# Kernel optimization log

Measured on AMD Instinct MI355X. Metric: run time of the kernel, lower is better.

The kernel has to match this reference:

```python
import jax, jax.numpy as jnp
import numpy as np

EPS_L2 = 1e-6
EPS_RMS = 1e-6

def _dw_causal(x, w):
    # depthwise causal conv: x [B,L,C], w [C,K] (torch Conv1d weight [C,1,K] squeezed)
    K = w.shape[1]
    L = x.shape[1]
    xp = jnp.pad(x, ((0, 0), (K - 1, 0), (0, 0)))
    out = jnp.zeros_like(x)
    for j in range(K):  # K=4, fixed small kernel
        out = out + w[:, j] * xp[:, j:j + L, :]
    return out

def _qkv_conv(x, dw, pw):
    # depthwise causal conv -> pointwise 1x1 conv -> SiLU
    return jax.nn.silu(_dw_causal(x, dw) @ pw.T)

def _l2n(x):
    return x / (jnp.linalg.norm(x, axis=-1, keepdims=True) + EPS_L2)

def setup_inputs() -> dict:
    key = jax.random.key(0)
    B, L, D, M, P, K = 2, 1024, 2048, 2048, 8, 4
    ks = jax.random.split(key, 16)
    inp = {}
    inp['x'] = jax.random.normal(ks[0], (B, L, D), dtype=jnp.float32)
    inp['Wq'] = jax.random.normal(ks[1], (M, D), dtype=jnp.float32) * 0.02
    inp['Wk'] = jax.random.normal(ks[2], (M, D), dtype=jnp.float32) * 0.02
    inp['Wv'] = jax.random.normal(ks[3], (M, D), dtype=jnp.float32) * 0.02
    inp['q_dw'] = jax.random.normal(ks[4], (M, K), dtype=jnp.float32) * 0.1
    inp['k_dw'] = jax.random.normal(ks[5], (M, K), dtype=jnp.float32) * 0.1
    inp['v_dw'] = jax.random.normal(ks[6], (M, K), dtype=jnp.float32) * 0.1
    inp['q_pw'] = jax.random.normal(ks[7], (M, M), dtype=jnp.float32) * 0.02
    inp['k_pw'] = jax.random.normal(ks[8], (M, M), dtype=jnp.float32) * 0.02
    inp['v_pw'] = jax.random.normal(ks[9], (M, M), dtype=jnp.float32) * 0.02
    inp['pk'] = jax.random.normal(ks[10], (P, M), dtype=jnp.float32) * 0.02
    inp['pv'] = jax.random.normal(ks[11], (P, M), dtype=jnp.float32) * 0.02
    inp['mlp_w1'] = jnp.eye(M, dtype=jnp.float32) * 0.1
    inp['mlp_w2'] = jnp.eye(M, dtype=jnp.float32) * 0.1
    inp['eta_w'] = jnp.zeros((1, D), dtype=jnp.float32)
    inp['eta_b'] = jnp.full((1,), 2.0, dtype=jnp.float32)
    inp['theta_w'] = jnp.zeros((1, D), dtype=jnp.float32)
    inp['theta_b'] = jnp.full((1,), -1.0, dtype=jnp.float32)
    inp['alpha_w'] = jnp.zeros((1, D), dtype=jnp.float32)
    inp['alpha_b'] = jnp.full((1,), -2.0, dtype=jnp.float32)
    inp['gate_w'] = jax.random.normal(ks[12], (M, M), dtype=jnp.float32) * 0.02
    inp['gate_b'] = jnp.zeros((M,), dtype=jnp.float32)
    inp['out_w'] = jax.random.normal(ks[13], (D, M), dtype=jnp.float32) * 0.02
    inp['ln_w'] = jnp.ones((D,), dtype=jnp.float32)
    inp['mem_state'] = jnp.zeros((M, M), dtype=jnp.float32)
    inp['sur_state'] = jnp.zeros((M, M), dtype=jnp.float32)
    return inp

def reference(x, Wq, Wk, Wv, q_dw, q_pw, k_dw, k_pw, v_dw, v_pw, pk, pv,
              mlp_w1, mlp_w2, eta_w, eta_b, theta_w, theta_b, alpha_w, alpha_b,
              gate_w, gate_b, out_w, ln_w, mem_state, sur_state):
    B, L, D = x.shape
    M = Wq.shape[0]
    P = pk.shape[0]
    # projections + causal depthwise-separable convs + SiLU
    q = _qkv_conv(x @ Wq.T, q_dw, q_pw)
    k = _qkv_conv(x @ Wk.T, k_dw, k_pw)
    v = _qkv_conv(x @ Wv.T, v_dw, v_pw)
    q = _l2n(q)
    k = _l2n(k)
    # data-dependent eta/theta/alpha from mean-pooled input, scalarized
    x_pooled = x.mean(axis=1)  # [B, D]
    eta = jax.nn.sigmoid(x_pooled @ eta_w.T + eta_b).mean()
    theta = jax.nn.sigmoid(x_pooled @ theta_w.T + theta_b).mean()
    alpha = jax.nn.sigmoid(x_pooled @ alpha_w.T + alpha_b).mean()
    # persistent memory tokens
    pk_n = _l2n(pk)
    k_wp = jnp.concatenate([jnp.broadcast_to(pk_n[None], (B, P, M)), k], axis=1)
    v_wp = jnp.concatenate([jnp.broadcast_to(pv[None], (B, P, M)), v], axis=1)
    # test-time memory update (torch.no_grad block -> stop_gradient)
    pred = jnp.einsum('blm,mh->blh', k, mem_state)
    err = v - pred
    momentary = jnp.einsum('bld,blh->dh', k, err) / (B * L)
    new_surprise = eta * sur_state + theta * momentary
    new_memory = (1.0 - alpha) * mem_state + new_surprise
    snapshot = jax.lax.stop_gradient(new_memory)
    # retrieval: linear memory + deep memory MLP
    linear_ret = jnp.einsum('blm,mh->blh', q, snapshot)
    mlp_ret = jax.nn.silu(q @ mlp_w1.T) @ mlp_w2.T
    retrieved = linear_ret + mlp_ret
    # causal attention with always-visible persistent tokens
    scores = jnp.einsum('blm,bpm->blp', q, k_wp) / jnp.sqrt(jnp.float32(M))
    col = jnp.arange(P + L)
    row = jnp.arange(L)
    mask = (col[None, :] < P) | ((col[None, :] - P) <= row[:, None])  # [L, P+L]
    scores = jnp.where(mask[None], scores, -jnp.inf)
    attn = jax.nn.softmax(scores.astype(jnp.float32), axis=-1).astype(x.dtype)
    context = jnp.einsum('blp,bpm->blm', attn, v_wp)
    retrieved = retrieved + context
    # gated output projection + residual + RMSNorm
    gate = jax.nn.sigmoid(retrieved @ gate_w.T + gate_b)
    out = x + (gate * retrieved) @ out_w.T
    rms = jnp.sqrt(jnp.mean(out * out, axis=-1, keepdims=True) + EPS_RMS)
    return (out / rms) * ln_w
```

## Files before the change

### kernel.cpp

```cpp
#include <hip/hip_runtime.h>
#include <hip/hip_bf16.h>


#define NROWS 2048
#define MD    2048
#define PL    1032
#define PLP   1152
#define NM    4194304

using bf16x8 = __attribute__((ext_vector_type(8))) __bf16;
using f32x4  = __attribute__((ext_vector_type(4))) float;
using u16x8  = __attribute__((ext_vector_type(8))) unsigned short;

__device__ __forceinline__ unsigned short f2bf(float f) {
    union { float f; unsigned int u; } c; c.f = f;
    unsigned int u = c.u;
    return (unsigned short)((u + 0x7fffu + ((u >> 16) & 1u)) >> 16);
}
__device__ __forceinline__ float bf2f(unsigned short h) {
    union { float f; unsigned int u; } c; c.u = ((unsigned int)h) << 16;
    return c.f;
}
__device__ __forceinline__ float ldf(const float* p) { return *p; }
__device__ __forceinline__ float ldf(const unsigned short* p) { return bf2f(*p); }
__device__ __forceinline__ float sigm(float x) { return 1.f / (1.f + __expf(-x)); }
__device__ __forceinline__ float silu(float x) { return x / (1.f + __expf(-x)); }

__device__ __forceinline__ float block_reduce_sum(float v) {
    __shared__ float ws[4];
    #pragma unroll
    for (int o = 32; o > 0; o >>= 1) v += __shfl_down(v, o);
    __syncthreads();
    if ((threadIdx.x & 63) == 0) ws[threadIdx.x >> 6] = v;
    __syncthreads();
    return (ws[0] + ws[1]) + (ws[2] + ws[3]);
}
__device__ __forceinline__ float block_reduce_max(float v) {
    __shared__ float wm[4];
    #pragma unroll
    for (int o = 32; o > 0; o >>= 1) v = fmaxf(v, __shfl_down(v, o));
    __syncthreads();
    if ((threadIdx.x & 63) == 0) wm[threadIdx.x >> 6] = v;
    __syncthreads();
    return fmaxf(fmaxf(wm[0], wm[1]), fmaxf(wm[2], wm[3]));
}

__device__ __forceinline__ void load_lds16(const unsigned short* g, unsigned short* l) {
    __builtin_amdgcn_global_load_lds(
        (const __attribute__((address_space(1))) unsigned int*)g,
        (__attribute__((address_space(3))) unsigned int*)l, 16, 0, 0);
}
__device__ __forceinline__ void raw_barrier() {
    __asm__ volatile("" ::: "memory");
    __builtin_amdgcn_s_barrier();
    __asm__ volatile("" ::: "memory");
}
__device__ __forceinline__ void epi_store(int epi, float* Cf, unsigned short* Ch,
                                          long off, float v) {
    if (epi == 0)      Cf[off] = v;
    else if (epi == 1) Cf[off] += v;
    else if (epi == 2) Ch[off] = f2bf(v);
    else               Ch[off] = f2bf(silu(v));
}

__global__ __launch_bounds__(256) void gemm_nt(
    const unsigned short* __restrict__ A, const unsigned short* __restrict__ Bm,
    void* __restrict__ Cv, int Mc, int K, long sA, long sB, long sCb, int epiPack)
{
    __shared__ unsigned short As[2][8192];
    __shared__ unsigned short Bs[2][4096];
    const int tid = threadIdx.x, lane = tid & 63, w = tid >> 6;
    const int l16 = lane & 15, quad = lane >> 4;
    const int wr = (w >> 1) * 64, wc = (w & 1) * 32;
    const long rowBase = (long)blockIdx.y * 128;
    const long colBase = (long)blockIdx.x * 64;
    const unsigned short* Ap = A + (long)blockIdx.z * sA;
    const unsigned short* Bp = Bm + (long)blockIdx.z * sB;
    const int epi = (epiPack >> (blockIdx.z * 4)) & 15;
    const int r8 = lane >> 3;
    const int cg = (lane & 7) ^ r8;

    const unsigned short* gA[4]; const unsigned short* gB[2];
    unsigned short* lA[4]; unsigned short* lB[2];
    #pragma unroll
    for (int t = 0; t < 4; ++t) {
        int ch = w * 4 + t;
        gA[t] = Ap + (rowBase + ch * 8 + r8) * (long)K + cg * 8;
        lA[t] = &As[0][ch * 512];
    }
    #pragma unroll
    for (int t = 0; t < 2; ++t) {
        int ch = w * 2 + t;
        gB[t] = Bp + (colBase + ch * 8 + r8) * (long)K + cg * 8;
        lB[t] = &Bs[0][ch * 512];
    }

    f32x4 acc[4][2] = {};
    #pragma unroll
    for (int t = 0; t < 4; ++t) { load_lds16(gA[t], lA[t]); gA[t] += 64; }
    #pragma unroll
    for (int t = 0; t < 2; ++t) { load_lds16(gB[t], lB[t]); gB[t] += 64; }

    const int nIter = K >> 6;
    for (int it = 0; it < nIter; ++it) {
        const int cb = it & 1;
        if (it + 1 < nIter) {
            const int nb = cb ^ 1;
            #pragma unroll
            for (int t = 0; t < 4; ++t) { load_lds16(gA[t], lA[t] + nb * 8192); gA[t] += 64; }
            #pragma unroll
            for (int t = 0; t < 2; ++t) { load_lds16(gB[t], lB[t] + nb * 4096); gB[t] += 64; }
            __builtin_amdgcn_s_waitcnt(0xF76);
        } else {
            __builtin_amdgcn_s_waitcnt(0xF70);
        }
        raw_barrier();
        const unsigned short* Ac = As[cb];
        const unsigned short* Bc = Bs[cb];
        #pragma unroll
        for (int ks = 0; ks < 2; ++ks) {
            const int cl = ((ks * 4 + quad) ^ (l16 & 7)) * 8;
            bf16x8 af[4], bfr[2];
            #pragma unroll
            for (int i = 0; i < 4; ++i)
                af[i] = *(const bf16x8*)&Ac[(wr + i * 16 + l16) * 64 + cl];
            #pragma unroll
            for (int j = 0; j < 2; ++j)
                bfr[j] = *(const bf16x8*)&Bc[(wc + j * 16 + l16) * 64 + cl];
            #pragma unroll
            for (int i = 0; i < 4; ++i)
                #pragma unroll
                for (int j = 0; j < 2; ++j)
                    acc[i][j] = __builtin_amdgcn_mfma_f32_16x16x32_bf16(af[i], bfr[j], acc[i][j], 0, 0, 0);
        }
        raw_barrier();
    }

    char* Cb = (char*)Cv + (long)blockIdx.z * sCb;
    float* Cf = (float*)Cb;
    unsigned short* Ch = (unsigned short*)Cb;
    #pragma unroll
    for (int i = 0; i < 4; ++i)
        #pragma unroll
        for (int r = 0; r < 4; ++r) {
            long gr = rowBase + wr + i * 16 + quad * 4 + r;
            #pragma unroll
            for (int j = 0; j < 2; ++j) {
                long gc = colBase + wc + j * 16 + l16;
                epi_store(epi, Cf, Ch, gr * (long)Mc + gc, acc[i][j][r]);
            }
        }
}

__global__ __launch_bounds__(256) void gemm_nt_big(
    const unsigned short* __restrict__ A, const unsigned short* __restrict__ Bm,
    void* __restrict__ Cv, int Mc, int K, long sA, long sB, long sCb, int epiPack)
{
    __shared__ unsigned short As[2][8192];
    __shared__ unsigned short Bs[2][8192];
    const int tid = threadIdx.x, lane = tid & 63, w = tid >> 6;
    const int l16 = lane & 15, quad = lane >> 4;
    const int wr = (w >> 1) * 64, wc = (w & 1) * 64;
    const long rowBase = (long)blockIdx.y * 128;
    const long colBase = (long)blockIdx.x * 128;
    const unsigned short* Ap = A + (long)blockIdx.z * sA;
    const unsigned short* Bp = Bm + (long)blockIdx.z * sB;
    const int epi = (epiPack >> (blockIdx.z * 4)) & 15;
    const int r8 = lane >> 3;
    const int cg = (lane & 7) ^ r8;

    const unsigned short* gA[4]; const unsigned short* gB[4];
    unsigned short* lA[4]; unsigned short* lB[4];
    #pragma unroll
    for (int t = 0; t < 4; ++t) {
        int ch = w * 4 + t;
        gA[t] = Ap + (rowBase + ch * 8 + r8) * (long)K + cg * 8;
        lA[t] = &As[0][ch * 512];
        gB[t] = Bp + (colBase + ch * 8 + r8) * (long)K + cg * 8;
        lB[t] = &Bs[0][ch * 512];
    }

    f32x4 acc[4][4] = {};
    #pragma unroll
    for (int t = 0; t < 4; ++t) { load_lds16(gA[t], lA[t]); gA[t] += 64; }
    #pragma unroll
    for (int t = 0; t < 4; ++t) { load_lds16(gB[t], lB[t]); gB[t] += 64; }

    const int nIter = K >> 6;
    for (int it = 0; it < nIter; ++it) {
        const int cb = it & 1;
        if (it + 1 < nIter) {
            const int nb = cb ^ 1;
            #pragma unroll
            for (int t = 0; t < 4; ++t) { load_lds16(gA[t], lA[t] + nb * 8192); gA[t] += 64; }
            #pragma unroll
            for (int t = 0; t < 4; ++t) { load_lds16(gB[t], lB[t] + nb * 8192); gB[t] += 64; }
            __builtin_amdgcn_s_waitcnt(0xF78);
        } else {
            __builtin_amdgcn_s_waitcnt(0xF70);
        }
        raw_barrier();
        const unsigned short* Ac = As[cb];
        const unsigned short* Bc = Bs[cb];
        #pragma unroll
        for (int ks = 0; ks < 2; ++ks) {
            const int cl = ((ks * 4 + quad) ^ (l16 & 7)) * 8;
            bf16x8 af[4], bfr[4];
            #pragma unroll
            for (int i = 0; i < 4; ++i)
                af[i] = *(const bf16x8*)&Ac[(wr + i * 16 + l16) * 64 + cl];
            #pragma unroll
            for (int j = 0; j < 4; ++j)
                bfr[j] = *(const bf16x8*)&Bc[(wc + j * 16 + l16) * 64 + cl];
            #pragma unroll
            for (int i = 0; i < 4; ++i)
                #pragma unroll
                for (int j = 0; j < 4; ++j)
                    acc[i][j] = __builtin_amdgcn_mfma_f32_16x16x32_bf16(af[i], bfr[j], acc[i][j], 0, 0, 0);
        }
        raw_barrier();
    }

    char* Cb = (char*)Cv + (long)blockIdx.z * sCb;
    float* Cf = (float*)Cb;
    unsigned short* Ch = (unsigned short*)Cb;
    #pragma unroll
    for (int i = 0; i < 4; ++i)
        #pragma unroll
        for (int r = 0; r < 4; ++r) {
            long gr = rowBase + wr + i * 16 + quad * 4 + r;
            #pragma unroll
            for (int j = 0; j < 4; ++j) {
                long gc = colBase + wc + j * 16 + l16;
                epi_store(epi, Cf, Ch, gr * (long)Mc + gc, acc[i][j][r]);
            }
        }
}

template <typename TS>
__global__ void k_transpose(const TS* __restrict__ src, unsigned short* __restrict__ dst,
                            int R, int C, int dstLd, int dstOff, long sSrc, long sDst)
{
    __shared__ float tile[32][33];
    const TS* sp = src + (long)blockIdx.z * sSrc;
    unsigned short* dp = dst + (long)blockIdx.z * sDst;
    int c0 = blockIdx.x * 32, r0 = blockIdx.y * 32;
    int tx = threadIdx.x, ty = threadIdx.y;
    #pragma unroll
    for (int i = 0; i < 4; ++i)
        tile[ty + i * 8][tx] = ldf(&sp[(long)(r0 + ty + i * 8) * C + c0 + tx]);
    __syncthreads();
    #pragma unroll
    for (int i = 0; i < 4; ++i)
        dp[(long)(c0 + ty + i * 8) * dstLd + dstOff + r0 + tx] = f2bf(tile[tx][ty + i * 8]);
}

__global__ void k_errT_kT(const unsigned short* __restrict__ vf, const float* __restrict__ pred,
                          const unsigned short* __restrict__ k_bf, unsigned short* __restrict__ eT)
{
    __shared__ float tile[32][33];
    int z = blockIdx.z;
    int c0 = blockIdx.x * 32, r0 = blockIdx.y * 32;
    int tx = threadIdx.x, ty = threadIdx.y;
    #pragma unroll
    for (int i = 0; i < 4; ++i) {
        long idx = (long)(r0 + ty + i * 8) * MD + c0 + tx;
        tile[ty + i * 8][tx] = (z == 0) ? (bf2f(vf[idx]) - pred[idx]) : bf2f(k_bf[idx]);
    }
    __syncthreads();
    unsigned short* dst = eT + (long)z * NM;
    #pragma unroll
    for (int i = 0; i < 4; ++i)
        dst[(long)(c0 + ty + i * 8) * MD + r0 + tx] = f2bf(tile[tx][ty + i * 8]);
}

__global__ void k_snapT(const float* __restrict__ mem, const float* __restrict__ sur,
                        const float* __restrict__ momT, const float* __restrict__ scal,
                        unsigned short* __restrict__ dst)
{
    __shared__ float tile[32][33];
    float eta = scal[0], theta = scal[1], alpha = scal[2];
    int h0 = blockIdx.y * 32, d0 = blockIdx.x * 32;
    int tx = threadIdx.x, ty = threadIdx.y;
    #pragma unroll
    for (int i = 0; i < 4; ++i) {
        long idx = (long)(d0 + ty + i * 8) * MD + h0 + tx;
        tile[ty + i * 8][tx] = (1.f - alpha) * mem[idx] + eta * sur[idx];
    }
    __syncthreads();
    #pragma unroll
    for (int i = 0; i < 4; ++i) {
        long oidx = (long)(h0 + ty + i * 8) * MD + d0 + tx;
        dst[oidx] = f2bf(tile[tx][ty + i * 8] + theta * (1.f / 2048.f) * momT[oidx]);
    }
}

__global__ void k_cvt_multi(const float* s0, const float* s1, const float* s2, const float* s3,
                            const float* s4, const float* s5, const float* s6, const float* s7,
                            unsigned short* d0, unsigned short* d1, unsigned short* d2, unsigned short* d3,
                            unsigned short* d4, unsigned short* d5, unsigned short* d6, unsigned short* d7)
{
    int seg = blockIdx.x >> 11;
    const float* s; unsigned short* d;
    switch (seg) {
        case 0: s = s0; d = d0; break;  case 1: s = s1; d = d1; break;
        case 2: s = s2; d = d2; break;  case 3: s = s3; d = d3; break;
        case 4: s = s4; d = d4; break;  case 5: s = s5; d = d5; break;
        case 6: s = s6; d = d6; break;  default: s = s7; d = d7; break;
    }
    long idx = ((long)(blockIdx.x & 2047) * 256 + threadIdx.x) * 8;
    float4 a = *(const float4*)(s + idx);
    float4 b = *(const float4*)(s + idx + 4);
    u16x8 o;
    o[0] = f2bf(a.x); o[1] = f2bf(a.y); o[2] = f2bf(a.z); o[3] = f2bf(a.w);
    o[4] = f2bf(b.x); o[5] = f2bf(b.y); o[6] = f2bf(b.z); o[7] = f2bf(b.w);
    *(u16x8*)(d + idx) = o;
}

__global__ void k_dwconv(const unsigned short* __restrict__ tproj,
                         const float* __restrict__ qdw, const float* __restrict__ kdw,
                         const float* __restrict__ vdw, unsigned short* __restrict__ conv)
{
    long u = (long)blockIdx.x * 256 + threadIdx.x;
    long flat = u * 8;
    int z = (int)(flat >> 22);
    int rem = (int)(flat & (NM - 1));
    int n = rem >> 11, m = rem & 2047;
    int l = n & 1023;
    const float* dw = (z == 0) ? qdw : (z == 1) ? kdw : vdw;
    const unsigned short* src = tproj + (long)n * 6144 + z * 2048 + m;
    float4 dwv[8];
    #pragma unroll
    for (int e = 0; e < 8; ++e) dwv[e] = *(const float4*)(dw + (m + e) * 4);
    float acc[8] = {};
    #pragma unroll
    for (int j = 0; j < 4; ++j) {
        int dl = j - 3;
        if (l + dl >= 0) {
            u16x8 r = *(const u16x8*)(src + (long)dl * 6144);
            #pragma unroll
            for (int e = 0; e < 8; ++e)
                acc[e] += ((const float*)&dwv[e])[j] * bf2f(r[e]);
        }
    }
    u16x8 o;
    #pragma unroll
    for (int e = 0; e < 8; ++e) o[e] = f2bf(acc[e]);
    *(u16x8*)(conv + (long)z * NM + (long)n * 2048 + m) = o;
}

__global__ void k_post_qkv(const float* __restrict__ t_big, unsigned short* __restrict__ q_bf,
                           unsigned short* __restrict__ k_bf, unsigned short* __restrict__ vf,
                           unsigned short* __restrict__ kwp)
{
    int bid = blockIdx.x, z = bid >> 11, n = bid & 2047;
    const float* row = t_big + (long)z * NM + (long)n * 2048;
    int t = threadIdx.x;
    float4 a = *(const float4*)(row + t * 8);
    float4 b = *(const float4*)(row + t * 8 + 4);
    float v[8] = {silu(a.x), silu(a.y), silu(a.z), silu(a.w),
                  silu(b.x), silu(b.y), silu(b.z), silu(b.w)};
    if (z == 2) {
        u16x8 o;
        #pragma unroll
        for (int e = 0; e < 8; ++e) o[e] = f2bf(v[e]);
        *(u16x8*)(vf + (long)n * 2048 + t * 8) = o;
        return;
    }
    float ss = 0.f;
    #pragma unroll
    for (int e = 0; e < 8; ++e) ss += v[e] * v[e];
    ss = block_reduce_sum(ss);
    float inv = 1.f / (sqrtf(ss) + 1e-6f);
    u16x8 o;
    #pragma unroll
    for (int e = 0; e < 8; ++e) o[e] = f2bf(v[e] * inv);
    if (z == 0) {
        *(u16x8*)(q_bf + (long)n * 2048 + t * 8) = o;
    } else {
        *(u16x8*)(k_bf + (long)n * 2048 + t * 8) = o;
        int bb = n >> 10, l = n & 1023;
        *(u16x8*)(kwp + ((long)bb * PLP + 8 + l) * MD + t * 8) = o;
    }
}

__global__ void k_misc(const float* __restrict__ pk, const float* __restrict__ pv,
                       unsigned short* __restrict__ kwp, unsigned short* __restrict__ vwpT)
{
    int bid = blockIdx.x, t = threadIdx.x;
    if (bid < 8) {
        const float* row = pk + bid * MD;
        float4 a = *(const float4*)(row + t * 8);
        float4 b = *(const float4*)(row + t * 8 + 4);
        float v[8] = {a.x, a.y, a.z, a.w, b.x, b.y, b.z, b.w};
        float ss = 0.f;
        #pragma unroll
        for (int e = 0; e < 8; ++e) ss += v[e] * v[e];
        ss = block_reduce_sum(ss);
        float inv = 1.f / (sqrtf(ss) + 1e-6f);
        u16x8 o;
        #pragma unroll
        for (int e = 0; e < 8; ++e) o[e] = f2bf(v[e] * inv);
        *(u16x8*)(kwp + (long)bid * MD + t * 8) = o;
        *(u16x8*)(kwp + (long)PLP * MD + (long)bid * MD + t * 8) = o;
    } else if (bid < 72) {
        int i = (bid - 8) * 256 + t;
        int m = i >> 3, pp = i & 7;
        unsigned short h = f2bf(pv[pp * MD + m]);
        vwpT[(long)m * PLP + pp] = h;
        vwpT[(long)MD * PLP + (long)m * PLP + pp] = h;
    } else if (bid < 312) {
        long flat = ((long)(bid - 72) * 256 + t) * 8;
        int b = (int)(flat / 245760);
        int r = (int)(flat % 245760);
        int j = 1032 + (r >> 11), m = r & 2047;
        u16x8 zz = {};
        *(u16x8*)(kwp + ((long)b * PLP + j) * MD + m) = zz;
    } else {
        long flat = ((long)(bid - 312) * 256 + t) * 8;
        int bm = (int)(flat / 120);
        int o = (int)(flat % 120);
        u16x8 zz = {};
        *(u16x8*)(vwpT + (long)bm * PLP + 1032 + o) = zz;
    }
}

__global__ void k_pooled(const float* __restrict__ x, const float* __restrict__ ew,
                         const float* __restrict__ tw, const float* __restrict__ aw,
                         float* __restrict__ dots) {
    int b = blockIdx.y;
    long base = (long)b * 1024 * MD;
    long start = (long)blockIdx.x * 8192;
    float s0 = 0, s1 = 0, s2 = 0;
    for (int s = 0; s < 32; ++s) {
        long f = start + threadIdx.x + (long)s * 256;
        float xv = x[base + f];
        int d = (int)(f & (MD - 1));
        s0 += xv * ew[d]; s1 += xv * tw[d]; s2 += xv * aw[d];
    }
    s0 = block_reduce_sum(s0);
    if (threadIdx.x == 0) atomicAdd(&dots[0 + b], s0);
    s1 = block_reduce_sum(s1);
    if (threadIdx.x == 0) atomicAdd(&dots[2 + b], s1);
    s2 = block_reduce_sum(s2);
    if (threadIdx.x == 0) atomicAdd(&dots[4 + b], s2);
}
__global__ void k_scal_fin(const float* __restrict__ dots, const float* __restrict__ eb,
                           const float* __restrict__ tb, const float* __restrict__ ab,
                           float* __restrict__ scal) {
    if (threadIdx.x == 0 && blockIdx.x == 0) {
        const float invL = 1.f / 1024.f;
        float e = 0, th = 0, al = 0;
        for (int b = 0; b < 2; ++b) {
            e  += sigm(dots[0 + b] * invL + eb[0]);
            th += sigm(dots[2 + b] * invL + tb[0]);
            al += sigm(dots[4 + b] * invL + ab[0]);
        }
        scal[0] = e * 0.5f; scal[1] = th * 0.5f; scal[2] = al * 0.5f;
    }
}

__global__ void k_addcvt(const float* __restrict__ a, const float* __restrict__ b,
                         unsigned short* __restrict__ o) {
    long i = ((long)blockIdx.x * 256 + threadIdx.x) * 8;
    float4 a0 = *(const float4*)(a + i), a1 = *(const float4*)(a + i + 4);
    float4 b0 = *(const float4*)(b + i), b1 = *(const float4*)(b + i + 4);
    u16x8 r;
    r[0] = f2bf(a0.x + b0.x); r[1] = f2bf(a0.y + b0.y); r[2] = f2bf(a0.z + b0.z); r[3] = f2bf(a0.w + b0.w);
    r[4] = f2bf(a1.x + b1.x); r[5] = f2bf(a1.y + b1.y); r[6] = f2bf(a1.z + b1.z); r[7] = f2bf(a1.w + b1.w);
    *(u16x8*)(o + i) = r;
}
__global__ void k_gate8(const float* __restrict__ pre, const float* __restrict__ gb,
                        const float* __restrict__ ret, const float* __restrict__ mlp2,
                        unsigned short* __restrict__ o) {
    long i = ((long)blockIdx.x * 256 + threadIdx.x) * 8;
    int m = (int)(i & (MD - 1));
    float4 p0 = *(const float4*)(pre + i),  p1 = *(const float4*)(pre + i + 4);
    float4 r0 = *(const float4*)(ret + i),  r1 = *(const float4*)(ret + i + 4);
    float4 q0 = *(const float4*)(mlp2 + i), q1 = *(const float4*)(mlp2 + i + 4);
    float4 g0 = *(const float4*)(gb + m),   g1 = *(const float4*)(gb + m + 4);
    u16x8 r;
    r[0] = f2bf(sigm(p0.x + g0.x) * (r0.x + q0.x));
    r[1] = f2bf(sigm(p0.y + g0.y) * (r0.y + q0.y));
    r[2] = f2bf(sigm(p0.z + g0.z) * (r0.z + q0.z));
    r[3] = f2bf(sigm(p0.w + g0.w) * (r0.w + q0.w));
    r[4] = f2bf(sigm(p1.x + g1.x) * (r1.x + q1.x));
    r[5] = f2bf(sigm(p1.y + g1.y) * (r1.y + q1.y));
    r[6] = f2bf(sigm(p1.z + g1.z) * (r1.z + q1.z));
    r[7] = f2bf(sigm(p1.w + g1.w) * (r1.w + q1.w));
    *(u16x8*)(o + i) = r;
}

__global__ void k_softmax(const float* __restrict__ S, unsigned short* __restrict__ attn) {
    int l = blockIdx.x, b = blockIdx.y;
    long base = ((long)b * 1024 + l) * PLP;
    int nvis = 8 + l + 1;
    const float scale = 0.022097086912079608f;
    int t = threadIdx.x;
    float vals[5];
    float mx = -1e30f;
    #pragma unroll
    for (int s = 0; s < 5; ++s) {
        int j = t + s * 256;
        float v = -1e30f;
        if (j < nvis) v = S[base + j] * scale;
        vals[s] = v;
        mx = fmaxf(mx, v);
    }
    mx = block_reduce_max(mx);
    float sum = 0.f;
    #pragma unroll
    for (int s = 0; s < 5; ++s) {
        int j = t + s * 256;
        float e = 0.f;
        if (j < nvis) e = __expf(vals[s] - mx);
        vals[s] = e; sum += e;
    }
    sum = block_reduce_sum(sum);
    float inv = 1.f / sum;
    #pragma unroll
    for (int s = 0; s < 5; ++s) {
        int j = t + s * 256;
        if (j < PLP) attn[base + j] = f2bf(vals[s] * inv);
    }
}

__global__ void k_final(const float* __restrict__ x, const float* __restrict__ y,
                        const float* __restrict__ lnw, float* __restrict__ out) {
    int n = blockIdx.x;
    long base = (long)n * MD;
    int t = threadIdx.x;
    float4 a0 = *(const float4*)(x + base + t * 8), a1 = *(const float4*)(x + base + t * 8 + 4);
    float4 b0 = *(const float4*)(y + base + t * 8), b1 = *(const float4*)(y + base + t * 8 + 4);
    float v[8] = {a0.x + b0.x, a0.y + b0.y, a0.z + b0.z, a0.w + b0.w,
                  a1.x + b1.x, a1.y + b1.y, a1.z + b1.z, a1.w + b1.w};
    float ss = 0.f;
    #pragma unroll
    for (int e = 0; e < 8; ++e) ss += v[e] * v[e];
    ss = block_reduce_sum(ss);
    float inv = rsqrtf(ss * (1.f / 2048.f) + 1e-6f);
    float4 w0 = *(const float4*)(lnw + t * 8), w1 = *(const float4*)(lnw + t * 8 + 4);
    float4 o0 = {v[0] * inv * w0.x, v[1] * inv * w0.y, v[2] * inv * w0.z, v[3] * inv * w0.w};
    float4 o1 = {v[4] * inv * w1.x, v[5] * inv * w1.y, v[6] * inv * w1.z, v[7] * inv * w1.w};
    *(float4*)(out + base + t * 8) = o0;
    *(float4*)(out + base + t * 8 + 4) = o1;
}

static inline void gemm64(hipStream_t st, const void* A, const void* B, void* C,
                          int Mc, int K, long sA, long sB, long sCb,
                          int gx, int gy, int gz, int epiPack) {
    hipLaunchKernelGGL(gemm_nt, dim3(gx, gy, gz), dim3(256), 0, st,
                       (const unsigned short*)A, (const unsigned short*)B, C,
                       Mc, K, sA, sB, sCb, epiPack);
}
static inline void gemm128(hipStream_t st, const void* A, const void* B, void* C,
                           int Mc, int K, long sA, long sB, long sCb,
                           int gx, int gy, int gz, int epiPack) {
    hipLaunchKernelGGL(gemm_nt_big, dim3(gx, gy, gz), dim3(256), 0, st,
                       (const unsigned short*)A, (const unsigned short*)B, C,
                       Mc, K, sA, sB, sCb, epiPack);
}

extern "C" void kernel_launch(void* const* d_in, const int* in_sizes, int n_in,
                              void* d_out, int out_size, void* d_ws, size_t ws_size,
                              hipStream_t stream) {
    const float* x    = (const float*)d_in[0];
    const float* Wq   = (const float*)d_in[1];
    const float* Wk   = (const float*)d_in[2];
    const float* Wv   = (const float*)d_in[3];
    const float* qdw  = (const float*)d_in[4];
    const float* kdw  = (const float*)d_in[5];
    const float* vdw  = (const float*)d_in[6];
    const float* qpw  = (const float*)d_in[7];
    const float* kpw  = (const float*)d_in[8];
    const float* vpw  = (const float*)d_in[9];
    const float* pk   = (const float*)d_in[10];
    const float* pv   = (const float*)d_in[11];
    const float* mw1  = (const float*)d_in[12];
    const float* mw2  = (const float*)d_in[13];
    const float* etaw = (const float*)d_in[14];
    const float* etab = (const float*)d_in[15];
    const float* thw  = (const float*)d_in[16];
    const float* thb  = (const float*)d_in[17];
    const float* alw  = (const float*)d_in[18];
    const float* alb  = (const float*)d_in[19];
    const float* gw   = (const float*)d_in[20];
    const float* gb   = (const float*)d_in[21];
    const float* ow   = (const float*)d_in[22];
    const float* lnw  = (const float*)d_in[23];
    const float* mem  = (const float*)d_in[24];
    const float* sur  = (const float*)d_in[25];
    float* out = (float*)d_out;

    char* ws = (char*)d_ws;
    const size_t MB = 1024 * 1024;
    float* dots = (float*)ws;
    float* scal = (float*)(ws + 1024);
    float*          t0f  = (float*)(ws + 4096);
    float*          t1f  = t0f + NM;
    float*          t2f  = t0f + 2 * NM;
    unsigned short* tproj = (unsigned short*)t0f;
    float*          retf = (float*)(ws + 4096 + 48 * MB);
    unsigned short* k_bf = (unsigned short*)(ws + 4096 + 64 * MB);
    unsigned short* q_bf = k_bf + NM;
    unsigned short* qc   = k_bf + 2 * NM;
    unsigned short* g_bf = k_bf;
    unsigned short* x_bf = (unsigned short*)(ws + 4096 + 88 * MB);
    unsigned short* vf   = x_bf;
    unsigned short* attn = x_bf;
    unsigned short* wQKV = (unsigned short*)(ws + 4096 + 96 * MB);
    unsigned short* conv = wQKV;
    unsigned short* kwp  = wQKV;
    unsigned short* vwpT = kwp + (long)2 * PLP * MD;
    unsigned short* wPW  = (unsigned short*)(ws + 4096 + 120 * MB);
    unsigned short* eT   = wPW;
    unsigned short* kT   = eT + NM;
    unsigned short* gw_bf = wPW;
    unsigned short* ow_bf = wPW + NM;
    unsigned short* wMem  = (unsigned short*)(ws + 4096 + 144 * MB);
    unsigned short* wMlp1 = wMem + NM;
    unsigned short* wSnap = wMem;
    unsigned short* wMlp2 = wMem + NM;

    const dim3 b256(256);
    const dim3 bT(32, 8);

    hipMemsetAsync(dots, 0, 256, stream);
    hipLaunchKernelGGL(k_pooled, dim3(256, 2), b256, 0, stream, x, etaw, thw, alw, dots);
    hipLaunchKernelGGL(k_scal_fin, dim3(1), dim3(64), 0, stream, dots, etab, thb, alb, scal);
    hipLaunchKernelGGL(k_cvt_multi, dim3(16384), b256, 0, stream,
                       x, Wq, Wk, Wv, qpw, kpw, vpw, mw1,
                       x_bf, wQKV, wQKV + NM, wQKV + 2 * (long)NM,
                       wPW, wPW + NM, wPW + 2 * (long)NM, wMlp1);
    hipLaunchKernelGGL(k_transpose<float>, dim3(64, 64, 1), bT, 0, stream,
                       mem, wMem, MD, MD, MD, 0, 0L, 0L);
    gemm128(stream, x_bf, wQKV, tproj, 6144, MD, 0, 0, 0, 48, 16, 1, 2);
    hipLaunchKernelGGL(k_dwconv, dim3(6144), b256, 0, stream, tproj, qdw, kdw, vdw, conv);
    gemm128(stream, conv, wPW, t0f, MD, MD, NM, NM, (long)NM * 4, 16, 16, 3, 0);
    hipLaunchKernelGGL(k_misc, dim3(552), b256, 0, stream, pk, pv, kwp, vwpT);
    hipLaunchKernelGGL(k_post_qkv, dim3(6144), b256, 0, stream, t0f, q_bf, k_bf, vf, kwp);
    hipLaunchKernelGGL(k_transpose<unsigned short>, dim3(64, 32, 2), bT, 0, stream,
                       vf, vwpT, 1024, MD, PLP, 8, (long)1024 * MD, (long)MD * PLP);
    gemm128(stream, k_bf, wMem, t0f, MD, MD, NM, NM,
            (long)((char*)qc - (char*)t0f), 16, 16, 2, 0x30);
    hipLaunchKernelGGL(k_errT_kT, dim3(64, 64, 2), bT, 0, stream, vf, t0f, k_bf, eT);
    gemm64(stream, eT, kT, t2f, MD, MD, 0, 0, 0, 32, 16, 1, 0);
    hipLaunchKernelGGL(k_snapT, dim3(64, 64), bT, 0, stream, mem, sur, t2f, scal, wSnap);
    hipLaunchKernelGGL(k_cvt_multi, dim3(6144), b256, 0, stream,
                       mw2, gw, ow, mw2, mw2, mw2, mw2, mw2,
                       wMlp2, gw_bf, ow_bf, wMlp2, wMlp2, wMlp2, wMlp2, wMlp2);
    gemm128(stream, q_bf, wSnap, retf, MD, MD, NM, NM,
            (long)((char*)t1f - (char*)retf), 16, 16, 2, 0);
    gemm64(stream, q_bf, kwp, t2f, PLP, MD,
           (long)1024 * MD, (long)PLP * MD, (long)1024 * PLP * 4, 18, 8, 2, 0);
    hipLaunchKernelGGL(k_softmax, dim3(1024, 2), b256, 0, stream, t2f, attn);
    gemm64(stream, attn, vwpT, retf, MD, PLP,
           (long)1024 * PLP, (long)MD * PLP, (long)1024 * MD * 4, 32, 8, 2, 0x11);
    hipLaunchKernelGGL(k_addcvt, dim3(2048), b256, 0, stream, retf, t1f, qc);
    hipLaunchKernelGGL(gemm_nt, dim3(32, 16, 1), dim3(256), 0, stream,
                       (const unsigned short*)qc, (const unsigned short*)gw_bf, (void*)t0f,
                       MD, MD, 0L, 0L, 0L, 0);
    hipLaunchKernelGGL(k_gate8, dim3(2048), b256, 0, stream, t0f, gb, retf, t1f, g_bf);
    gemm64(stream, g_bf, ow_bf, t0f, MD, MD, 0, 0, 0, 32, 16, 1, 0);
    hipLaunchKernelGGL(k_final, dim3(2048), b256, 0, stream, x, t0f, lnw, out);
}
```

Measured before the change: 782.4 us.

## Replace 128x128 GEMM with 256x256 tile, 512-thread ping-pong pipelined kernel

Replaces the 128x128-tile, 256-thread double-buffered GEMM with a 256x256-tile, 512-thread kernel. Each K step is split into four phases that interleave LDS reads, staggered global-to-LDS staging of A and B, and MFMA bursts raised with s_setprio. The goal is more operand reuse per byte loaded and better overlap of memory with compute on the large 2048/6144-wide GEMMs. In exchange, grids shrink to 64–192 blocks, which may leave many of the device's CUs idle, and register and LDS pressure rise.

```diff
diff --git a/kernel.cpp b/kernel.cpp
--- a/kernel.cpp
+++ b/kernel.cpp
@@ -152,72 +152,121 @@
         }
 }
 
-__global__ __launch_bounds__(256) void gemm_nt_big(
+#define G256_RD_A(p)                                                            \
+    _Pragma("unroll") for (int fr = 0; fr < 2; ++fr)                            \
+    _Pragma("unroll") for (int ks = 0; ks < 2; ++ks)                            \
+        af[fr][ks] = *(const bf16x8*)&Ac[(wr + ((p) * 2 + fr) * 16 + l16) * 64  \
+                                         + ((ks * 4 + quad) ^ (l16 & 7)) * 8];
+#define G256_MFMA(p)                                                            \
+    __builtin_amdgcn_s_setprio(1);                                              \
+    _Pragma("unroll") for (int ks = 0; ks < 2; ++ks)                            \
+    _Pragma("unroll") for (int fr = 0; fr < 2; ++fr)                            \
+    _Pragma("unroll") for (int fc = 0; fc < 4; ++fc)                            \
+        acc[(p) * 2 + fr][fc] = __builtin_amdgcn_mfma_f32_16x16x32_bf16(        \
+            af[fr][ks], bfr[fc][ks], acc[(p) * 2 + fr][fc], 0, 0, 0);           \
+    __builtin_amdgcn_s_setprio(0);
+#define G256_STG_A(h)                                                           \
+    do { load_lds16(gA[h][0], &Anx[lofs[h][0]]); gA[h][0] += 64;                \
+         load_lds16(gA[h][1], &Anx[lofs[h][1]]); gA[h][1] += 64; } while (0)
+#define G256_STG_B(h)                                                           \
+    do { load_lds16(gB[h][0], &Bnx[lofs[h][0]]); gB[h][0] += 64;                \
+         load_lds16(gB[h][1], &Bnx[lofs[h][1]]); gB[h][1] += 64; } while (0)
+
+__global__ __launch_bounds__(512, 2) void gemm_nt_256(
     const unsigned short* __restrict__ A, const unsigned short* __restrict__ Bm,
     void* __restrict__ Cv, int Mc, int K, long sA, long sB, long sCb, int epiPack)
 {
-    __shared__ unsigned short As[2][8192];
-    __shared__ unsigned short Bs[2][8192];
+    __shared__ unsigned short As[2][16384];
+    __shared__ unsigned short Bs[2][16384];
     const int tid = threadIdx.x, lane = tid & 63, w = tid >> 6;
     const int l16 = lane & 15, quad = lane >> 4;
-    const int wr = (w >> 1) * 64, wc = (w & 1) * 64;
-    const long rowBase = (long)blockIdx.y * 128;
-    const long colBase = (long)blockIdx.x * 128;
+    const int wr = (w >> 2) * 128, wc = (w & 3) * 64;
+    const long rowBase = (long)blockIdx.y * 256;
+    const long colBase = (long)blockIdx.x * 256;
     const unsigned short* Ap = A + (long)blockIdx.z * sA;
     const unsigned short* Bp = Bm + (long)blockIdx.z * sB;
     const int epi = (epiPack >> (blockIdx.z * 4)) & 15;
     const int r8 = lane >> 3;
     const int cg = (lane & 7) ^ r8;
 
-    const unsigned short* gA[4]; const unsigned short* gB[4];
-    unsigned short* lA[4]; unsigned short* lB[4];
-    #pragma unroll
-    for (int t = 0; t < 4; ++t) {
-        int ch = w * 4 + t;
-        gA[t] = Ap + (rowBase + ch * 8 + r8) * (long)K + cg * 8;
-        lA[t] = &As[0][ch * 512];
-        gB[t] = Bp + (colBase + ch * 8 + r8) * (long)K + cg * 8;
-        lB[t] = &Bs[0][ch * 512];
-    }
-
-    f32x4 acc[4][4] = {};
-    #pragma unroll
-    for (int t = 0; t < 4; ++t) { load_lds16(gA[t], lA[t]); gA[t] += 64; }
-    #pragma unroll
-    for (int t = 0; t < 4; ++t) { load_lds16(gB[t], lB[t]); gB[t] += 64; }
-
-    const int nIter = K >> 6;
-    for (int it = 0; it < nIter; ++it) {
-        const int cb = it & 1;
-        if (it + 1 < nIter) {
-            const int nb = cb ^ 1;
-            #pragma unroll
-            for (int t = 0; t < 4; ++t) { load_lds16(gA[t], lA[t] + nb * 8192); gA[t] += 64; }
-            #pragma unroll
-            for (int t = 0; t < 4; ++t) { load_lds16(gB[t], lB[t] + nb * 8192); gB[t] += 64; }
-            __builtin_amdgcn_s_waitcnt(0xF78);
-        } else {
-            __builtin_amdgcn_s_waitcnt(0xF70);
+    const unsigned short* gA[2][2]; const unsigned short* gB[2][2];
+    int lofs[2][2];
+    #pragma unroll
+    for (int h = 0; h < 2; ++h)
+        #pragma unroll
+        for (int j = 0; j < 2; ++j) {
+            const int rowOff = h * 128 + j * 64 + w * 8 + r8;
+            gA[h][j] = Ap + (rowBase + rowOff) * (long)K + cg * 8;
+            gB[h][j] = Bp + (colBase + rowOff) * (long)K + cg * 8;
+            lofs[h][j] = (h * 128 + j * 64 + w * 8) * 64;
         }
-        raw_barrier();
+
+    const int nT = K >> 6;
+    f32x4 acc[8][4] = {};
+
+    #pragma unroll
+    for (int h = 0; h < 2; ++h)
+        #pragma unroll
+        for (int j = 0; j < 2; ++j) { load_lds16(gA[h][j], &As[0][lofs[h][j]]); gA[h][j] += 64; }
+    #pragma unroll
+    for (int h = 0; h < 2; ++h)
+        #pragma unroll
+        for (int j = 0; j < 2; ++j) { load_lds16(gB[h][j], &Bs[0][lofs[h][j]]); gB[h][j] += 64; }
+    if (nT > 1) {
+        #pragma unroll
+        for (int h = 0; h < 2; ++h)
+            #pragma unroll
+            for (int j = 0; j < 2; ++j) { load_lds16(gB[h][j], &Bs[1][lofs[h][j]]); gB[h][j] += 64; }
+        __builtin_amdgcn_s_waitcnt(0x0F74);
+    } else {
+        __builtin_amdgcn_s_waitcnt(0x0F70);
+    }
+    raw_barrier();
+
+    for (int t = 0; t < nT; ++t) {
+        const int cb = t & 1;
         const unsigned short* Ac = As[cb];
         const unsigned short* Bc = Bs[cb];
-        #pragma unroll
-        for (int ks = 0; ks < 2; ++ks) {
-            const int cl = ((ks * 4 + quad) ^ (l16 & 7)) * 8;
-            bf16x8 af[4], bfr[4];
-            #pragma unroll
-            for (int i = 0; i < 4; ++i)
-                af[i] = *(const bf16x8*)&Ac[(wr + i * 16 + l16) * 64 + cl];
-            #pragma unroll
-            for (int j = 0; j < 4; ++j)
-                bfr[j] = *(const bf16x8*)&Bc[(wc + j * 16 + l16) * 64 + cl];
-            #pragma unroll
-            for (int i = 0; i < 4; ++i)
-                #pragma unroll
-                for (int j = 0; j < 4; ++j)
-                    acc[i][j] = __builtin_amdgcn_mfma_f32_16x16x32_bf16(af[i], bfr[j], acc[i][j], 0, 0, 0);
+        unsigned short* Anx = As[cb ^ 1];
+        unsigned short* Bnx = Bs[cb];
+        const bool stA = (t + 1 < nT);
+        const bool stB = (t + 2 < nT);
+        bf16x8 bfr[4][2];
+        bf16x8 af[2][2];
+
+        #pragma unroll
+        for (int fc = 0; fc < 4; ++fc)
+            #pragma unroll
+            for (int ks = 0; ks < 2; ++ks)
+                bfr[fc][ks] = *(const bf16x8*)&Bc[(wc + fc * 16 + l16) * 64
+                                                 + ((ks * 4 + quad) ^ (l16 & 7)) * 8];
+        G256_RD_A(0)
+        if (stA) G256_STG_A(0);
+        raw_barrier();
+        G256_MFMA(0)
+        raw_barrier();
+
+        G256_RD_A(1)
+        if (stA) G256_STG_A(1);
+        raw_barrier();
+        G256_MFMA(1)
+        raw_barrier();
+
+        G256_RD_A(2)
+        if (stB) G256_STG_B(0);
+        raw_barrier();
+        G256_MFMA(2)
+        raw_barrier();
+
+        G256_RD_A(3)
+        if (stB) {
+            G256_STG_B(1);
+            __builtin_amdgcn_s_waitcnt(0x0F74);
+        } else {
+            __builtin_amdgcn_s_waitcnt(0x0F70);
         }
+        raw_barrier();
+        G256_MFMA(3)
         raw_barrier();
     }
 
@@ -225,7 +274,7 @@
     float* Cf = (float*)Cb;
     unsigned short* Ch = (unsigned short*)Cb;
     #pragma unroll
-    for (int i = 0; i < 4; ++i)
+    for (int i = 0; i < 8; ++i)
         #pragma unroll
         for (int r = 0; r < 4; ++r) {
             long gr = rowBase + wr + i * 16 + quad * 4 + r;
@@ -553,10 +602,10 @@
                        (const unsigned short*)A, (const unsigned short*)B, C,
                        Mc, K, sA, sB, sCb, epiPack);
 }
-static inline void gemm128(hipStream_t st, const void* A, const void* B, void* C,
+static inline void gemm256(hipStream_t st, const void* A, const void* B, void* C,
                            int Mc, int K, long sA, long sB, long sCb,
                            int gx, int gy, int gz, int epiPack) {
-    hipLaunchKernelGGL(gemm_nt_big, dim3(gx, gy, gz), dim3(256), 0, st,
+    hipLaunchKernelGGL(gemm_nt_256, dim3(gx, gy, gz), dim3(512), 0, st,
                        (const unsigned short*)A, (const unsigned short*)B, C,
                        Mc, K, sA, sB, sCb, epiPack);
 }
@@ -634,32 +683,30 @@
                        wPW, wPW + NM, wPW + 2 * (long)NM, wMlp1);
     hipLaunchKernelGGL(k_transpose<float>, dim3(64, 64, 1), bT, 0, stream,
                        mem, wMem, MD, MD, MD, 0, 0L, 0L);
-    gemm128(stream, x_bf, wQKV, tproj, 6144, MD, 0, 0, 0, 48, 16, 1, 2);
+    gemm256(stream, x_bf, wQKV, tproj, 6144, MD, 0, 0, 0, 24, 8, 1, 2);
     hipLaunchKernelGGL(k_dwconv, dim3(6144), b256, 0, stream, tproj, qdw, kdw, vdw, conv);
-    gemm128(stream, conv, wPW, t0f, MD, MD, NM, NM, (long)NM * 4, 16, 16, 3, 0);
+    gemm256(stream, conv, wPW, t0f, MD, MD, NM, NM, (long)NM * 4, 8, 8, 3, 0);
     hipLaunchKernelGGL(k_misc, dim3(552), b256, 0, stream, pk, pv, kwp, vwpT);
     hipLaunchKernelGGL(k_post_qkv, dim3(6144), b256, 0, stream, t0f, q_bf, k_bf, vf, kwp);
     hipLaunchKernelGGL(k_transpose<unsigned short>, dim3(64, 32, 2), bT, 0, stream,
                        vf, vwpT, 1024, MD, PLP, 8, (long)1024 * MD, (long)MD * PLP);
-    gemm128(stream, k_bf, wMem, t0f, MD, MD, NM, NM,
-            (long)((char*)qc - (char*)t0f), 16, 16, 2, 0x30);
+    gemm256(stream, k_bf, wMem, t0f, MD, MD, NM, NM,
+            (long)((char*)qc - (char*)t0f), 8, 8, 2, 0x30);
     hipLaunchKernelGGL(k_errT_kT, dim3(64, 64, 2), bT, 0, stream, vf, t0f, k_bf, eT);
     gemm64(stream, eT, kT, t2f, MD, MD, 0, 0, 0, 32, 16, 1, 0);
     hipLaunchKernelGGL(k_snapT, dim3(64, 64), bT, 0, stream, mem, sur, t2f, scal, wSnap);
     hipLaunchKernelGGL(k_cvt_multi, dim3(6144), b256, 0, stream,
                        mw2, gw, ow, mw2, mw2, mw2, mw2, mw2,
                        wMlp2, gw_bf, ow_bf, wMlp2, wMlp2, wMlp2, wMlp2, wMlp2);
-    gemm128(stream, q_bf, wSnap, retf, MD, MD, NM, NM,
-            (long)((char*)t1f - (char*)retf), 16, 16, 2, 0);
+    gemm256(stream, q_bf, wSnap, retf, MD, MD, NM, NM,
+            (long)((char*)t1f - (char*)retf), 8, 8, 2, 0);
     gemm64(stream, q_bf, kwp, t2f, PLP, MD,
            (long)1024 * MD, (long)PLP * MD, (long)1024 * PLP * 4, 18, 8, 2, 0);
     hipLaunchKernelGGL(k_softmax, dim3(1024, 2), b256, 0, stream, t2f, attn);
     gemm64(stream, attn, vwpT, retf, MD, PLP,
            (long)1024 * PLP, (long)MD * PLP, (long)1024 * MD * 4, 32, 8, 2, 0x11);
     hipLaunchKernelGGL(k_addcvt, dim3(2048), b256, 0, stream, retf, t1f, qc);
-    hipLaunchKernelGGL(gemm_nt, dim3(32, 16, 1), dim3(256), 0, stream,
-                       (const unsigned short*)qc, (const unsigned short*)gw_bf, (void*)t0f,
-                       MD, MD, 0L, 0L, 0L, 0);
+    gemm64(stream, qc, gw_bf, t0f, MD, MD, 0, 0, 0, 32, 16, 1, 0);
     hipLaunchKernelGGL(k_gate8, dim3(2048), b256, 0, stream, t0f, gb, retf, t1f, g_bf);
     gemm64(stream, g_bf, ow_bf, t0f, MD, MD, 0, 0, 0, 32, 16, 1, 0);
     hipLaunchKernelGGL(k_final, dim3(2048), b256, 0, stream, x, t0f, lnw, out);
```

Result: slower. 816.1 us (+4.3%).
